# Kernel tuning notes

Measured on AMD Instinct MI355X. Metric: run time of the kernel, lower is better.

Reference implementation:

```python
import jax, jax.numpy as jnp
import numpy as np

IN_DIM, HIDDEN, OUT_DIM = 784, 2048, 10
BATCH = 16384
KEEP = 0.1  # 1 - sparsity


def setup_inputs() -> dict:
    key = jax.random.key(0)
    ks = jax.random.split(key, 16)
    s1 = 1.0 / np.sqrt(IN_DIM)
    sh = 1.0 / np.sqrt(HIDDEN)
    inp = {
        "x": jax.random.normal(ks[0], (BATCH, IN_DIM), dtype=jnp.float32),
        # weights stored as (out, in) like nn.Linear
        "W1": jax.random.uniform(ks[1], (HIDDEN, IN_DIM), jnp.float32, -s1, s1),
        "b1": jax.random.uniform(ks[2], (HIDDEN,), jnp.float32, -s1, s1),
        "W2": jax.random.uniform(ks[3], (HIDDEN, HIDDEN), jnp.float32, -sh, sh),
        "b2": jax.random.uniform(ks[4], (HIDDEN,), jnp.float32, -sh, sh),
        "W3": jax.random.uniform(ks[5], (HIDDEN, HIDDEN), jnp.float32, -sh, sh),
        "b3": jax.random.uniform(ks[6], (HIDDEN,), jnp.float32, -sh, sh),
        "W4": jax.random.uniform(ks[7], (HIDDEN, HIDDEN), jnp.float32, -sh, sh),
        "b4": jax.random.uniform(ks[8], (HIDDEN,), jnp.float32, -sh, sh),
        "W5": jax.random.uniform(ks[9], (OUT_DIM, HIDDEN), jnp.float32, -sh, sh),
        "b5": jax.random.uniform(ks[10], (OUT_DIM,), jnp.float32, -sh, sh),
        "m1": jax.random.bernoulli(ks[11], KEEP, (HIDDEN, IN_DIM)),
        "m2": jax.random.bernoulli(ks[12], KEEP, (HIDDEN, HIDDEN)),
        "m3": jax.random.bernoulli(ks[13], KEEP, (HIDDEN, HIDDEN)),
        "m4": jax.random.bernoulli(ks[14], KEEP, (HIDDEN, HIDDEN)),
    }
    return inp


def _sparse_linear(x, W, b, m):
    # masked linear: y = x @ (W*m)^T + b
    Wm = W * m.astype(W.dtype)
    return x @ Wm.T + b


def reference(x, W1, b1, W2, b2, W3, b3, W4, b4, W5, b5, m1, m2, m3, m4):
    h = x.reshape(x.shape[0], -1)
    h = jax.nn.relu(_sparse_linear(h, W1, b1, m1))
    h = jax.nn.relu(_sparse_linear(h, W2, b2, m2))
    h = jax.nn.relu(_sparse_linear(h, W3, b3, m3))
    h = jax.nn.relu(_sparse_linear(h, W4, b4, m4))
    return h @ W5.T + b5
```

## Files before the change

### kernel.cpp

```cpp
#include <hip/hip_runtime.h>
#include <hip/hip_bf16.h>
#include <hip/hip_fp16.h>

#define BATCH 16384
#define HID   2048
#define IND   784
#define INDP  896
#define OUTD  10

typedef _Float16 f16;
typedef __attribute__((ext_vector_type(8))) _Float16 f16x8;
typedef __attribute__((ext_vector_type(4))) float f32x4;

__global__ void mask_detect(const unsigned char* __restrict__ p, int nbytes,
                            int* __restrict__ flags) {
    int acc = 0;
    for (int i = blockIdx.x * blockDim.x + threadIdx.x; i < nbytes;
         i += gridDim.x * blockDim.x) {
        unsigned char b = p[i];
        if (b > 1) acc |= 2;
        else if (b != 0 && (i & 3) != 0) acc |= 1;
    }
    if (acc) atomicOr(flags, acc);
}

__global__ void prep_cast(const float* __restrict__ W,
                          const void* __restrict__ Mk,
                          const int* __restrict__ flags,
                          f16* __restrict__ out,
                          int rin, int kin, int kout, int total) {
    int idx = blockIdx.x * blockDim.x + threadIdx.x;
    if (idx >= total) return;
    int r = idx / kout, c = idx - r * kout;
    float v = 0.f;
    if (r < rin && c < kin) {
        v = W[(size_t)r * kin + c];
        if (Mk) {
            size_t mi = (size_t)r * kin + c;
            bool byteMode = (*flags == 1);
            bool keep = byteMode ? (((const unsigned char*)Mk)[mi] != 0)
                                 : (((const unsigned int*)Mk)[mi] != 0u);
            if (!keep) v = 0.f;
        }
    }
    out[idx] = (f16)v;
}

__device__ __forceinline__ void gload_lds16(const f16* g, f16* l) {
    __builtin_amdgcn_global_load_lds(
        (const __attribute__((address_space(1))) unsigned int*)g,
        (__attribute__((address_space(3))) unsigned int*)l,
        16, 0, 0);
}

#define BAR()   __builtin_amdgcn_s_barrier()
#define SCHED() __builtin_amdgcn_sched_barrier(0)
#define WAITV4() asm volatile("s_waitcnt vmcnt(4)" ::: "memory")
#define WAITL0() asm volatile("s_waitcnt lgkmcnt(0)" ::: "memory")

template<bool RELU>
__global__ __launch_bounds__(512, 2) void gemm8p(
    const f16* __restrict__ A, const f16* __restrict__ B,
    const float* __restrict__ bias, f16* __restrict__ C,
    int N, int K) {
    __shared__ f16 As[2 * 2 * 256 * 32];
    __shared__ f16 Bs[2 * 2 * 256 * 32];

    int nbn = N >> 8;
    int nwg = gridDim.x;
    int cpx = nwg >> 3;
    int bid = blockIdx.x;
    int swz = (bid & 7) * cpx + (bid >> 3);
    int bm = swz / nbn, bn = swz % nbn;

    int tid = threadIdx.x;
    int w = tid >> 6, lane = tid & 63;
    int wr = w >> 2, wc = w & 3;
    int l15 = lane & 15, l4 = lane >> 4;

    const f16* Ag = A + (size_t)bm * 256 * K;
    const f16* Bg = B + (size_t)bn * 256 * K;

    int r0 = tid >> 2, s0 = tid & 3;
    int c0 = (s0 ^ ((r0 >> 1) & 3)) * 8;
    int ldsw0 = (w * 64) * 8;
    int ldsw1 = (512 + w * 64) * 8;

    auto stageA = [&](int buf, int ks, int tk) {
        const f16* s = Ag + (size_t)r0 * K + tk * 64 + ks * 32 + c0;
        gload_lds16(s, As + (buf * 2 + ks) * 8192 + ldsw0);
        const f16* s2 = Ag + (size_t)(128 + r0) * K + tk * 64 + ks * 32 + c0;
        gload_lds16(s2, As + (buf * 2 + ks) * 8192 + ldsw1);
    };
    auto stageB = [&](int buf, int ks, int tk) {
        const f16* s = Bg + (size_t)r0 * K + tk * 64 + ks * 32 + c0;
        gload_lds16(s, Bs + (buf * 2 + ks) * 8192 + ldsw0);
        const f16* s2 = Bg + (size_t)(128 + r0) * K + tk * 64 + ks * 32 + c0;
        gload_lds16(s2, Bs + (buf * 2 + ks) * 8192 + ldsw1);
    };

    int rsw = (l4 ^ ((l15 >> 1) & 3)) * 8;
    auto ldA = [&](f16x8 (&af)[4], int buf, int ks, int mh) {
        int base = (buf * 2 + ks) * 8192;
        #pragma unroll
        for (int m = 0; m < 4; ++m) {
            int row = wr * 128 + (mh * 4 + m) * 16 + l15;
            af[m] = *(const f16x8*)(As + base + row * 32 + rsw);
        }
    };
    auto ldB = [&](f16x8 (&bf)[4], int buf, int ks) {
        int base = (buf * 2 + ks) * 8192;
        #pragma unroll
        for (int n = 0; n < 4; ++n) {
            int row = wc * 64 + n * 16 + l15;
            bf[n] = *(const f16x8*)(Bs + base + row * 32 + rsw);
        }
    };

    f32x4 acc[8][4] = {};
    auto mma = [&](f16x8 (&af)[4], f16x8 (&bf)[4], int mh) {
        __builtin_amdgcn_s_setprio(1);
        #pragma unroll
        for (int m = 0; m < 4; ++m)
            #pragma unroll
            for (int n = 0; n < 4; ++n)
                acc[mh * 4 + m][n] = __builtin_amdgcn_mfma_f32_16x16x32_f16(
                    af[m], bf[n], acc[mh * 4 + m][n], 0, 0, 0);
        __builtin_amdgcn_s_setprio(0);
    };

    int NT = K >> 6, NI = NT >> 1;

    stageA(0, 0, 0); stageB(0, 0, 0); stageA(0, 1, 0); stageB(0, 1, 0);
    stageA(1, 0, 1); stageB(1, 0, 1);
    WAITV4(); SCHED(); BAR();

    for (int it = 0; it < NI; ++it) {
        int t1 = 2 * it + 1, t2 = 2 * it + 2, t3 = 2 * it + 3;
        if (t2 >= NT) t2 = 0;
        if (t3 >= NT) t3 = 0;
        f16x8 a0[4], a1[4], b0[4], b1[4];

        ldA(a0, 0, 0, 0); ldB(b0, 0, 0); stageA(1, 1, t1);
        SCHED(); BAR(); WAITL0(); SCHED();
        mma(a0, b0, 0); BAR();
        ldA(a1, 0, 0, 1); stageB(1, 1, t1);
        SCHED(); BAR(); WAITL0(); SCHED();
        mma(a1, b0, 1); BAR();
        ldA(a0, 0, 1, 0); ldB(b1, 0, 1); stageA(0, 0, t2);
        SCHED(); BAR(); WAITL0(); SCHED();
        mma(a0, b1, 0); BAR();
        ldA(a1, 0, 1, 1); stageB(0, 0, t2);
        SCHED(); BAR(); WAITL0(); SCHED();
        mma(a1, b1, 1); WAITV4(); SCHED(); BAR();
        ldA(a0, 1, 0, 0); ldB(b0, 1, 0); stageA(0, 1, t2);
        SCHED(); BAR(); WAITL0(); SCHED();
        mma(a0, b0, 0); BAR();
        ldA(a1, 1, 0, 1); stageB(0, 1, t2);
        SCHED(); BAR(); WAITL0(); SCHED();
        mma(a1, b0, 1); BAR();
        ldA(a0, 1, 1, 0); ldB(b1, 1, 1); stageA(1, 0, t3);
        SCHED(); BAR(); WAITL0(); SCHED();
        mma(a0, b1, 0); BAR();
        ldA(a1, 1, 1, 1); stageB(1, 0, t3);
        SCHED(); BAR(); WAITL0(); SCHED();
        mma(a1, b1, 1); WAITV4(); SCHED(); BAR();
    }

    #pragma unroll
    for (int nf = 0; nf < 4; ++nf) {
        int j = bn * 256 + wc * 64 + nf * 16 + l15;
        float bv = bias[j];
        #pragma unroll
        for (int mf = 0; mf < 8; ++mf) {
            int i0 = bm * 256 + wr * 128 + mf * 16 + l4 * 4;
            #pragma unroll
            for (int r = 0; r < 4; ++r) {
                float v = acc[mf][nf][r] + bv;
                if (RELU) v = fmaxf(v, 0.f);
                C[(size_t)(i0 + r) * N + j] = (f16)v;
            }
        }
    }
}

__global__ __launch_bounds__(256, 3) void gemm_head(
    const f16* __restrict__ A, const f16* __restrict__ B,
    const float* __restrict__ bias, float* __restrict__ C,
    int K, int Nout) {
    __shared__ f16 As[128 * 64];
    __shared__ f16 Bs[128 * 64];
    int bm = blockIdx.x;
    int t = threadIdx.x;
    int w = t >> 6, lane = t & 63;
    int wm = w >> 1, wn = w & 1;
    int l15 = lane & 15, l4 = lane >> 4;
    const f16* Ag = A + (size_t)bm * 128 * K;
    const f16* Bg = B;
    int rr = w * 8 + (lane >> 3);
    int cc = (lane & 7) * 8;
    f32x4 acc[4][4] = {};
    for (int k0 = 0; k0 < K; k0 += 64) {
        #pragma unroll
        for (int i = 0; i < 4; ++i)
            gload_lds16(Ag + (size_t)(i * 32 + rr) * K + k0 + cc, As + i * 2048 + w * 512);
        #pragma unroll
        for (int i = 0; i < 4; ++i)
            gload_lds16(Bg + (size_t)(i * 32 + rr) * K + k0 + cc, Bs + i * 2048 + w * 512);
        __syncthreads();
        #pragma unroll
        for (int ks = 0; ks < 2; ++ks) {
            f16x8 af[4], bfr[4];
            #pragma unroll
            for (int m = 0; m < 4; ++m)
                af[m] = *(const f16x8*)(As + (wm * 64 + m * 16 + l15) * 64 + ks * 32 + l4 * 8);
            #pragma unroll
            for (int n = 0; n < 4; ++n)
                bfr[n] = *(const f16x8*)(Bs + (wn * 64 + n * 16 + l15) * 64 + ks * 32 + l4 * 8);
            #pragma unroll
            for (int m = 0; m < 4; ++m)
                #pragma unroll
                for (int n = 0; n < 4; ++n)
                    acc[m][n] = __builtin_amdgcn_mfma_f32_16x16x32_f16(af[m], bfr[n], acc[m][n], 0, 0, 0);
        }
        __syncthreads();
    }
    #pragma unroll
    for (int n = 0; n < 4; ++n) {
        int j = wn * 64 + n * 16 + l15;
        bool jok = j < Nout;
        float bv = jok ? bias[j] : 0.f;
        #pragma unroll
        for (int m = 0; m < 4; ++m) {
            int i0 = bm * 128 + wm * 64 + m * 16 + l4 * 4;
            #pragma unroll
            for (int r = 0; r < 4; ++r) {
                if (jok) C[(size_t)(i0 + r) * Nout + j] = acc[m][n][r] + bv;
            }
        }
    }
}

extern "C" void kernel_launch(void* const* d_in, const int* in_sizes, int n_in,
                              void* d_out, int out_size, void* d_ws, size_t ws_size,
                              hipStream_t stream) {
    const float* x  = (const float*)d_in[0];
    const float* W1 = (const float*)d_in[1];
    const float* b1 = (const float*)d_in[2];
    const float* W2 = (const float*)d_in[3];
    const float* b2 = (const float*)d_in[4];
    const float* W3 = (const float*)d_in[5];
    const float* b3 = (const float*)d_in[6];
    const float* W4 = (const float*)d_in[7];
    const float* b4 = (const float*)d_in[8];
    const float* W5 = (const float*)d_in[9];
    const float* b5 = (const float*)d_in[10];
    const void* m1 = d_in[11];
    const void* m2 = d_in[12];
    const void* m3 = d_in[13];
    const void* m4 = d_in[14];

    char* ws = (char*)d_ws;
    size_t off = 0;
    auto alloc = [&](size_t b) { char* p = ws + off; off += (b + 255) & ~(size_t)255; return p; };
    f16* xb  = (f16*)alloc((size_t)BATCH * INDP * 2);
    f16* w1b = (f16*)alloc((size_t)HID * INDP * 2);
    f16* w2b = (f16*)alloc((size_t)HID * HID * 2);
    f16* w3b = (f16*)alloc((size_t)HID * HID * 2);
    f16* w4b = (f16*)alloc((size_t)HID * HID * 2);
    f16* w5b = (f16*)alloc((size_t)128 * HID * 2);
    f16* h1  = (f16*)alloc((size_t)BATCH * HID * 2);
    f16* h2  = (f16*)alloc((size_t)BATCH * HID * 2);
    int* flags = (int*)alloc(256);

    hipMemsetAsync(flags, 0, sizeof(int), stream);
    mask_detect<<<64, 256, 0, stream>>>((const unsigned char*)m1, 262144, flags);

    auto prep = [&](const float* src, const void* mk, f16* dst,
                    int rin, int kin, int kout, int rout) {
        int total = rout * kout;
        prep_cast<<<(total + 255) / 256, 256, 0, stream>>>(src, mk, flags, dst,
                                                           rin, kin, kout, total);
    };
    prep(x,  nullptr, xb,  BATCH, IND, INDP, BATCH);
    prep(W1, m1,      w1b, HID,   IND, INDP, HID);
    prep(W2, m2,      w2b, HID,   HID, HID,  HID);
    prep(W3, m3,      w3b, HID,   HID, HID,  HID);
    prep(W4, m4,      w4b, HID,   HID, HID,  HID);
    prep(W5, nullptr, w5b, OUTD,  HID, HID,  128);

    int g8 = (BATCH / 256) * (HID / 256);
    gemm8p<true><<<g8, 512, 0, stream>>>(xb, w1b, b1, h1, HID, INDP);
    gemm8p<true><<<g8, 512, 0, stream>>>(h1, w2b, b2, h2, HID, HID);
    gemm8p<true><<<g8, 512, 0, stream>>>(h2, w3b, b3, h1, HID, HID);
    gemm8p<true><<<g8, 512, 0, stream>>>(h1, w4b, b4, h2, HID, HID);
    gemm_head<<<BATCH / 128, 256, 0, stream>>>(h2, w5b, b5, (float*)d_out, HID, OUTD);
}
```

Measured before the change: 558.3 us.

## Software-pipeline LDS fragment loads with MFMA using double-buffered registers

Restructures the GEMM main loop so the LDS-to-register fragment loads for the next sub-step are issued before the MFMAs of the current sub-step, ping-ponging between two register sets (A0/A1, B0/B1). It drops the per-phase pair of barriers to one per phase and adds a prologue that preloads the first fragments. The aim is to hide LDS read latency behind matrix math and cut synchronisation stalls. In exchange it uses more registers under the 512x2 launch bounds and needs careful vmcnt/barrier ordering to avoid LDS hazards.

```diff
diff --git a/kernel.cpp b/kernel.cpp
--- a/kernel.cpp
+++ b/kernel.cpp
@@ -53,9 +53,10 @@
         16, 0, 0);
 }
 
-#define BAR()   __builtin_amdgcn_s_barrier()
-#define SCHED() __builtin_amdgcn_sched_barrier(0)
+#define BAR()    __builtin_amdgcn_s_barrier()
+#define SCHED()  __builtin_amdgcn_sched_barrier(0)
 #define WAITV4() asm volatile("s_waitcnt vmcnt(4)" ::: "memory")
+#define WAITV8() asm volatile("s_waitcnt vmcnt(8)" ::: "memory")
 #define WAITL0() asm volatile("s_waitcnt lgkmcnt(0)" ::: "memory")
 
 template<bool RELU>
@@ -131,40 +132,43 @@
 
     int NT = K >> 6, NI = NT >> 1;
 
+    f16x8 A0[4], A1[4], B0[4], B1[4];
+
     stageA(0, 0, 0); stageB(0, 0, 0); stageA(0, 1, 0); stageB(0, 1, 0);
     stageA(1, 0, 1); stageB(1, 0, 1);
-    WAITV4(); SCHED(); BAR();
+    WAITV8(); SCHED(); BAR();
+    ldA(A0, 0, 0, 0); ldB(B0, 0, 0);
+    WAITL0(); SCHED();
 
     for (int it = 0; it < NI; ++it) {
         int t1 = 2 * it + 1, t2 = 2 * it + 2, t3 = 2 * it + 3;
         if (t2 >= NT) t2 = 0;
         if (t3 >= NT) t3 = 0;
-        f16x8 a0[4], a1[4], b0[4], b1[4];
-
-        ldA(a0, 0, 0, 0); ldB(b0, 0, 0); stageA(1, 1, t1);
-        SCHED(); BAR(); WAITL0(); SCHED();
-        mma(a0, b0, 0); BAR();
-        ldA(a1, 0, 0, 1); stageB(1, 1, t1);
-        SCHED(); BAR(); WAITL0(); SCHED();
-        mma(a1, b0, 1); BAR();
-        ldA(a0, 0, 1, 0); ldB(b1, 0, 1); stageA(0, 0, t2);
-        SCHED(); BAR(); WAITL0(); SCHED();
-        mma(a0, b1, 0); BAR();
-        ldA(a1, 0, 1, 1); stageB(0, 0, t2);
-        SCHED(); BAR(); WAITL0(); SCHED();
-        mma(a1, b1, 1); WAITV4(); SCHED(); BAR();
-        ldA(a0, 1, 0, 0); ldB(b0, 1, 0); stageA(0, 1, t2);
-        SCHED(); BAR(); WAITL0(); SCHED();
-        mma(a0, b0, 0); BAR();
-        ldA(a1, 1, 0, 1); stageB(0, 1, t2);
-        SCHED(); BAR(); WAITL0(); SCHED();
-        mma(a1, b0, 1); BAR();
-        ldA(a0, 1, 1, 0); ldB(b1, 1, 1); stageA(1, 0, t3);
-        SCHED(); BAR(); WAITL0(); SCHED();
-        mma(a0, b1, 0); BAR();
-        ldA(a1, 1, 1, 1); stageB(1, 0, t3);
-        SCHED(); BAR(); WAITL0(); SCHED();
-        mma(a1, b1, 1); WAITV4(); SCHED(); BAR();
+
+        ldA(A1, 0, 0, 1); stageA(1, 1, t1); SCHED();
+        mma(A0, B0, 0);
+        WAITL0(); WAITV4(); SCHED(); BAR();
+        ldA(A0, 0, 1, 0); ldB(B1, 0, 1); stageB(1, 1, t1); SCHED();
+        mma(A1, B0, 1);
+        WAITL0(); SCHED(); BAR();
+        ldA(A1, 0, 1, 1); stageA(0, 0, t2); SCHED();
+        mma(A0, B1, 0);
+        WAITL0(); WAITV4(); SCHED(); BAR();
+        ldA(A0, 1, 0, 0); ldB(B0, 1, 0); stageB(0, 0, t2); SCHED();
+        mma(A1, B1, 1);
+        WAITL0(); SCHED(); BAR();
+        ldA(A1, 1, 0, 1); stageA(0, 1, t2); SCHED();
+        mma(A0, B0, 0);
+        WAITL0(); WAITV4(); SCHED(); BAR();
+        ldA(A0, 1, 1, 0); ldB(B1, 1, 1); stageB(0, 1, t2); SCHED();
+        mma(A1, B0, 1);
+        WAITL0(); SCHED(); BAR();
+        ldA(A1, 1, 1, 1); stageA(1, 0, t3); SCHED();
+        mma(A0, B1, 0);
+        WAITL0(); WAITV4(); SCHED(); BAR();
+        ldA(A0, 0, 0, 0); ldB(B0, 0, 0); stageB(1, 0, t3); SCHED();
+        mma(A1, B1, 1);
+        WAITL0(); SCHED(); BAR();
     }
 
     #pragma unroll
```

Measured after the change: 562.4 us. No clear change (+0.7%).
